# Kernel optimization log

Hardware: AMD Instinct MI355X
Metric: run time of the kernel (lower is better)

The kernel has to match this reference:

```python
import jax, jax.numpy as jnp
import numpy as np

jax.config.update("jax_enable_x64", True)

MANT_SCALE = 8388608.0  # 2**23


def _decode_fp32_bits(bits):
    """[..., 32] {0,1} pulses (MSB-first IEEE-754 float32) -> float64 value."""
    f64 = jnp.float64
    sign = 1.0 - 2.0 * bits[..., 0].astype(f64)
    e = jnp.einsum('...j,j->...', bits[..., 1:9].astype(f64),
                   jnp.exp2(jnp.arange(7, -1, -1, dtype=f64)))
    frac = jnp.einsum('...j,j->...', bits[..., 9:32].astype(f64),
                      jnp.exp2(-jnp.arange(1, 24, dtype=f64)))
    normal = sign * jnp.exp2(e - 127.0) * (1.0 + frac)
    subnorm = sign * jnp.exp2(-126.0) * frac
    return jnp.where(e > 0, normal, subnorm)


def _encode_fp32_bits(y):
    """float64 value already on the fp32 grid -> [..., 32] {0,1} pulses (MSB-first)."""
    f64 = jnp.float64
    sbit = (y < 0).astype(f64)
    a = jnp.abs(y)
    e = jnp.clip(jnp.floor(jnp.log2(jnp.where(a > 0, a, 1.0))), -126.0, 127.0)
    eb = jnp.where(a > 0, e + 127.0, 0.0)          # biased exponent, 0 for zero/subnormal
    frac = jnp.where(eb > 0, a * jnp.exp2(-e) - 1.0, a * jnp.exp2(126.0))
    mant = frac * MANT_SCALE                        # exact integer for fp32-grid y
    ebits = jnp.mod(jnp.floor(eb[..., None] * jnp.exp2(-jnp.arange(7, -1, -1, dtype=f64))), 2.0)
    mbits = jnp.mod(jnp.floor(mant[..., None] * jnp.exp2(-jnp.arange(22, -1, -1, dtype=f64))), 2.0)
    bits = jnp.concatenate([sbit[..., None], ebits, mbits], axis=-1)
    return jnp.where((a > 0)[..., None], bits, 0.0).astype(jnp.float32)


def setup_inputs() -> dict:
    rng = np.random.default_rng(0)
    vals = (rng.standard_normal((1, 2048, 1024)) * 2.0).astype(np.float32)
    words = vals.view(np.uint32)
    shifts = np.arange(31, -1, -1, dtype=np.uint32)
    bits = ((words[..., None] >> shifts) & np.uint32(1)).astype(np.float32)
    return {"x": jnp.asarray(bits)}


def reference(x):
    # GELU(x) ~= x * sigmoid(1.702 * x), all intermediates in fp64 (as the
    # gate-level pipeline does), final result rounded once to fp32 bits.
    xv = _decode_fp32_bits(x)
    y64 = xv * jax.nn.sigmoid(1.702 * xv)
    y32 = y64.astype(jnp.float32).astype(jnp.float64)  # FP64 -> FP32 rounding
    return _encode_fp32_bits(y32)
```

## Files before the change

kernel.cpp:

```cpp
#include <hip/hip_runtime.h>
#include <math.h>


#define LN2C 0x1.62e42fefa39efp-1

typedef unsigned int u32x4 __attribute__((ext_vector_type(4)));

__global__ __launch_bounds__(256) void spike_gelu_kernel(
    const u32x4* __restrict__ in, u32x4* __restrict__ out, int n_vals) {
#pragma clang fp contract(off)
  const double LN2 = LN2C;
  __shared__ double Wdec[8];
  __shared__ double Lms[23];
  __shared__ double E1t[256];
  __shared__ double Vdec[23];
  __shared__ double P2t[254];
  __shared__ uint32_t etab[256];

  const int tid = threadIdx.x;
  if (tid < 8) Wdec[tid] = exp((double)(7 - tid) * LN2);
  if (tid >= 31 && tid < 54) Lms[tid - 31] = exp((double)(31 - tid) * LN2);
  __syncthreads();

  const int lane = tid & 63;
  const int vbase = blockIdx.x * 512 + (tid >> 6) * 128;
  const int n_chunks = n_vals * 8;
  const int cbase = vbase * 8 + lane;
  u32x4 bufA[8];
#pragma unroll
  for (int i = 0; i < 8; ++i) {
    int g = cbase + i * 64;
    u32x4 b = {0u, 0u, 0u, 0u};
    if (g < n_chunks) b = __builtin_nontemporal_load(&in[g]);
    bufA[i] = b;
  }

  if (tid == 0) {
    E1t[0] = exp(-126.0 * LN2);
  } else {
    double e_c = 0.0;
#pragma unroll
    for (int j = 0; j < 8; ++j)
      if ((tid >> (7 - j)) & 1) e_c = e_c + Wdec[j];
    E1t[tid] = exp((e_c - 127.0) * LN2);
  }
  if (tid < 23) Vdec[tid] = exp((double)(-1 - tid) * LN2);
  if (tid < 254) P2t[tid] = exp((double)(126 - tid) * LN2);
  if (tid >= 1 && tid < 255) {
    double eb = (double)tid;
    uint32_t r = 0;
#pragma unroll
    for (int sc = 7; sc >= 0; --sc) {
      double f = floor(eb * Lms[sc]);
      double md = f - 2.0 * floor(0.5 * f);
      r |= ((uint32_t)md) << (23 + sc);
    }
    etab[tid] = r;
  } else {
    etab[tid] = 0u;
  }
  __syncthreads();

  u32x4 bufB[8];
#pragma unroll
  for (int i = 0; i < 8; ++i) {
    int g = cbase + 512 + i * 64;
    u32x4 b = {0u, 0u, 0u, 0u};
    if (g < n_chunks) b = __builtin_nontemporal_load(&in[g]);
    bufB[i] = b;
  }

  const int nibshift = 28 - 4 * (lane & 7);
  const int keep = lane & 7;
  uint32_t w0 = 0u, w1 = 0u;
#pragma unroll
  for (int i = 0; i < 8; ++i) {
    u32x4 b = bufA[i];
    uint32_t p = (((((b.x >> 23) & 1u) << 3) | (((b.y >> 23) & 1u) << 2) |
                   (((b.z >> 23) & 1u) << 1) | ((b.w >> 23) & 1u)))
                 << nibshift;
    p |= __shfl_xor(p, 1);
    p |= __shfl_xor(p, 2);
    p |= __shfl_xor(p, 4);
    if (keep == i) w0 = p;
  }
#pragma unroll
  for (int i = 0; i < 8; ++i) {
    u32x4 b = bufB[i];
    uint32_t p = (((((b.x >> 23) & 1u) << 3) | (((b.y >> 23) & 1u) << 2) |
                   (((b.z >> 23) & 1u) << 1) | ((b.w >> 23) & 1u)))
                 << nibshift;
    p |= __shfl_xor(p, 1);
    p |= __shfl_xor(p, 2);
    p |= __shfl_xor(p, 4);
    if (keep == i) w1 = p;
  }

  const int v0 = vbase + (lane & 7) * 8 + (lane >> 3);
  const int v1 = v0 + 64;
  const bool ok0 = v0 < n_vals, ok1 = v1 < n_vals;

  double f0 = 0.0, f1 = 0.0;
#pragma unroll
  for (int j = 0; j < 23; ++j) {
    double vj = Vdec[j];
    if ((w0 >> (22 - j)) & 1u) f0 = f0 + vj;
    if ((w1 >> (22 - j)) & 1u) f1 = f1 + vj;
  }
  uint32_t ei0 = (w0 >> 23) & 0xFFu, ei1 = (w1 >> 23) & 0xFFu;
  double sg0 = (w0 >> 31) ? -1.0 : 1.0, sg1 = (w1 >> 31) ? -1.0 : 1.0;
  double fa0 = ei0 ? (1.0 + f0) : f0, fa1 = ei1 ? (1.0 + f1) : f1;
  double x0 = (sg0 * E1t[ei0]) * fa0, x1 = (sg1 * E1t[ei1]) * fa1;

  double t0 = 1.702 * x0, t1 = 1.702 * x1;
  double e0v = exp(-t0), e1v = exp(-t1);
  double s0 = 1.0 / (1.0 + e0v), s1 = 1.0 / (1.0 + e1v);
  double y0 = x0 * s0, y1 = x1 * s1;
  float yf0 = (float)y0, yf1 = (float)y1;
  double yd0 = (double)yf0, yd1 = (double)yf1;

  double a0 = fabs(yd0), a1 = fabs(yd1);
  uint32_t yb0 = __float_as_uint(yf0), yb1 = __float_as_uint(yf1);
  uint32_t Ef0 = (yb0 >> 23) & 0xFFu, Ef1 = (yb1 >> 23) & 0xFFu;
  uint32_t mbf0 = yb0 & 0x7FFFFFu, mbf1 = yb1 & 0x7FFFFFu;
  int e00 = (Ef0 == 0u) ? -126 : (int)Ef0 - 127;
  int e01 = (Ef1 == 0u) ? -126 : (int)Ef1 - 127;
  bool pw0 = ok0 && (a0 > 0.0) && (Ef0 != 0u) && (mbf0 == 0u);
  bool pw1 = ok1 && (a1 > 0.0) && (Ef1 != 0u) && (mbf1 == 0u);
  if (__builtin_expect(pw0 || pw1, 0)) {
    if (pw0) {
      double e0 = floor(log(a0) / LN2);
      e00 = (int)fmin(fmax(e0, -126.0), 127.0);
    }
    if (pw1) {
      double e0 = floor(log(a1) / LN2);
      e01 = (int)fmin(fmax(e0, -126.0), 127.0);
    }
  }
  double p20 = P2t[e00 + 126], p21 = P2t[e01 + 126];
  double m10 = a0 * p20, m11 = a1 * p21;
  double mant0 = (m10 - 1.0) * 8388608.0;
  double mant1 = (m11 - 1.0) * 8388608.0;
  int M0 = (int)rint(mant0), M1 = (int)rint(mant1);
  uint32_t mb0 = ((uint32_t)M0) & 0x7FFFFFu, mb1 = ((uint32_t)M1) & 0x7FFFFFu;
  int T0 = M0 ? __builtin_ctz((uint32_t)M0) : 23;
  int T1 = M1 ? __builtin_ctz((uint32_t)M1) : 23;
  int L0 = T0 < 22 ? T0 : 22, L1 = T1 < 22 ? T1 : 22;
  int Lmax = L0 > L1 ? L0 : L1;
  for (int sc = 0; sc <= Lmax; ++sc) {
    double lm = Lms[sc];
    if (sc <= L0) {
      double f = floor(mant0 * lm);
      mb0 = (mb0 & ~(1u << sc)) | (((uint32_t)(((int)f) & 1)) << sc);
    }
    if (sc <= L1) {
      double f = floor(mant1 * lm);
      mb1 = (mb1 & ~(1u << sc)) | (((uint32_t)(((int)f) & 1)) << sc);
    }
  }
  uint32_t ob0 = (yb0 & 0x80000000u) | etab[e00 + 127] | mb0;
  uint32_t ob1 = (yb1 & 0x80000000u) | etab[e01 + 127] | mb1;
  ob0 = (ok0 && a0 > 0.0) ? ob0 : 0u;
  ob1 = (ok1 && a1 > 0.0) ? ob1 : 0u;

#pragma unroll
  for (int i = 0; i < 8; ++i) {
    int g0 = cbase + i * 64;
    int g1 = g0 + 512;
    int src = (lane & 56) + i;
    uint32_t wa = __shfl(ob0, src);
    uint32_t wb = __shfl(ob1, src);
    int base = 31 - 4 * (lane & 7);
    if (g0 < n_chunks) {
      u32x4 o;
      o.x = ((wa >> base) & 1u) * 0x3F800000u;
      o.y = ((wa >> (base - 1)) & 1u) * 0x3F800000u;
      o.z = ((wa >> (base - 2)) & 1u) * 0x3F800000u;
      o.w = ((wa >> (base - 3)) & 1u) * 0x3F800000u;
      __builtin_nontemporal_store(o, &out[g0]);
    }
    if (g1 < n_chunks) {
      u32x4 o;
      o.x = ((wb >> base) & 1u) * 0x3F800000u;
      o.y = ((wb >> (base - 1)) & 1u) * 0x3F800000u;
      o.z = ((wb >> (base - 2)) & 1u) * 0x3F800000u;
      o.w = ((wb >> (base - 3)) & 1u) * 0x3F800000u;
      __builtin_nontemporal_store(o, &out[g1]);
    }
  }
}

extern "C" void kernel_launch(void* const* d_in, const int* in_sizes, int n_in,
                              void* d_out, int out_size, void* d_ws, size_t ws_size,
                              hipStream_t stream) {
  int n_vals = in_sizes[0] / 32;
  int grid = (n_vals + 511) / 512;
  spike_gelu_kernel<<<grid, 256, 0, stream>>>(
      (const u32x4*)d_in[0], (u32x4*)d_out, n_vals);
}
```

Measured before the change: 419.3 us.

## Convert to persistent grid-stride kernel with software-pipelined prefetch of next tile

```diff
diff --git a/kernel.cpp b/kernel.cpp
--- a/kernel.cpp
+++ b/kernel.cpp
@@ -6,8 +6,38 @@
 
 typedef unsigned int u32x4 __attribute__((ext_vector_type(4)));
 
+__device__ __forceinline__ void load_group(const u32x4* __restrict__ in,
+                                           int cb, int n_chunks,
+                                           u32x4 (&B)[8]) {
+#pragma unroll
+  for (int i = 0; i < 8; ++i) {
+    int g = cb + i * 64;
+    u32x4 b = {0u, 0u, 0u, 0u};
+    if (g < n_chunks) b = __builtin_nontemporal_load(&in[g]);
+    B[i] = b;
+  }
+}
+
+__device__ __forceinline__ uint32_t pack_group(const u32x4 (&B)[8],
+                                               int nibshift, int keep) {
+  uint32_t w = 0;
+#pragma unroll
+  for (int i = 0; i < 8; ++i) {
+    u32x4 b = B[i];
+    uint32_t p = (((((b.x >> 23) & 1u) << 3) | (((b.y >> 23) & 1u) << 2) |
+                   (((b.z >> 23) & 1u) << 1) | ((b.w >> 23) & 1u)))
+                 << nibshift;
+    p |= __shfl_xor(p, 1);
+    p |= __shfl_xor(p, 2);
+    p |= __shfl_xor(p, 4);
+    if (keep == i) w = p;
+  }
+  return w;
+}
+
 __global__ __launch_bounds__(256) void spike_gelu_kernel(
-    const u32x4* __restrict__ in, u32x4* __restrict__ out, int n_vals) {
+    const u32x4* __restrict__ in, u32x4* __restrict__ out,
+    int n_vals, int n_tiles) {
 #pragma clang fp contract(off)
   const double LN2 = LN2C;
   __shared__ double Wdec[8];
@@ -18,23 +48,21 @@
   __shared__ uint32_t etab[256];
 
   const int tid = threadIdx.x;
+  const int lane = tid & 63;
+  const int wid = tid >> 6;
+  const int n_chunks = n_vals * 8;
+  const int nibshift = 28 - 4 * (lane & 7);
+  const int keep = lane & 7;
+  const int tstep = gridDim.x;
+
+  int tile = blockIdx.x;
+  u32x4 A[8], Bb[8];
+
+  load_group(in, tile * 4096 + wid * 1024 + lane, n_chunks, A);
+
   if (tid < 8) Wdec[tid] = exp((double)(7 - tid) * LN2);
   if (tid >= 31 && tid < 54) Lms[tid - 31] = exp((double)(31 - tid) * LN2);
   __syncthreads();
-
-  const int lane = tid & 63;
-  const int vbase = blockIdx.x * 512 + (tid >> 6) * 128;
-  const int n_chunks = n_vals * 8;
-  const int cbase = vbase * 8 + lane;
-  u32x4 bufA[8];
-#pragma unroll
-  for (int i = 0; i < 8; ++i) {
-    int g = cbase + i * 64;
-    u32x4 b = {0u, 0u, 0u, 0u};
-    if (g < n_chunks) b = __builtin_nontemporal_load(&in[g]);
-    bufA[i] = b;
-  }
-
   if (tid == 0) {
     E1t[0] = exp(-126.0 * LN2);
   } else {
@@ -61,132 +89,123 @@
   }
   __syncthreads();
 
-  u32x4 bufB[8];
-#pragma unroll
-  for (int i = 0; i < 8; ++i) {
-    int g = cbase + 512 + i * 64;
-    u32x4 b = {0u, 0u, 0u, 0u};
-    if (g < n_chunks) b = __builtin_nontemporal_load(&in[g]);
-    bufB[i] = b;
-  }
-
-  const int nibshift = 28 - 4 * (lane & 7);
-  const int keep = lane & 7;
-  uint32_t w0 = 0u, w1 = 0u;
-#pragma unroll
-  for (int i = 0; i < 8; ++i) {
-    u32x4 b = bufA[i];
-    uint32_t p = (((((b.x >> 23) & 1u) << 3) | (((b.y >> 23) & 1u) << 2) |
-                   (((b.z >> 23) & 1u) << 1) | ((b.w >> 23) & 1u)))
-                 << nibshift;
-    p |= __shfl_xor(p, 1);
-    p |= __shfl_xor(p, 2);
-    p |= __shfl_xor(p, 4);
-    if (keep == i) w0 = p;
-  }
-#pragma unroll
-  for (int i = 0; i < 8; ++i) {
-    u32x4 b = bufB[i];
-    uint32_t p = (((((b.x >> 23) & 1u) << 3) | (((b.y >> 23) & 1u) << 2) |
-                   (((b.z >> 23) & 1u) << 1) | ((b.w >> 23) & 1u)))
-                 << nibshift;
-    p |= __shfl_xor(p, 1);
-    p |= __shfl_xor(p, 2);
-    p |= __shfl_xor(p, 4);
-    if (keep == i) w1 = p;
-  }
-
-  const int v0 = vbase + (lane & 7) * 8 + (lane >> 3);
-  const int v1 = v0 + 64;
-  const bool ok0 = v0 < n_vals, ok1 = v1 < n_vals;
-
-  double f0 = 0.0, f1 = 0.0;
-#pragma unroll
-  for (int j = 0; j < 23; ++j) {
-    double vj = Vdec[j];
-    if ((w0 >> (22 - j)) & 1u) f0 = f0 + vj;
-    if ((w1 >> (22 - j)) & 1u) f1 = f1 + vj;
-  }
-  uint32_t ei0 = (w0 >> 23) & 0xFFu, ei1 = (w1 >> 23) & 0xFFu;
-  double sg0 = (w0 >> 31) ? -1.0 : 1.0, sg1 = (w1 >> 31) ? -1.0 : 1.0;
-  double fa0 = ei0 ? (1.0 + f0) : f0, fa1 = ei1 ? (1.0 + f1) : f1;
-  double x0 = (sg0 * E1t[ei0]) * fa0, x1 = (sg1 * E1t[ei1]) * fa1;
-
-  double t0 = 1.702 * x0, t1 = 1.702 * x1;
-  double e0v = exp(-t0), e1v = exp(-t1);
-  double s0 = 1.0 / (1.0 + e0v), s1 = 1.0 / (1.0 + e1v);
-  double y0 = x0 * s0, y1 = x1 * s1;
-  float yf0 = (float)y0, yf1 = (float)y1;
-  double yd0 = (double)yf0, yd1 = (double)yf1;
-
-  double a0 = fabs(yd0), a1 = fabs(yd1);
-  uint32_t yb0 = __float_as_uint(yf0), yb1 = __float_as_uint(yf1);
-  uint32_t Ef0 = (yb0 >> 23) & 0xFFu, Ef1 = (yb1 >> 23) & 0xFFu;
-  uint32_t mbf0 = yb0 & 0x7FFFFFu, mbf1 = yb1 & 0x7FFFFFu;
-  int e00 = (Ef0 == 0u) ? -126 : (int)Ef0 - 127;
-  int e01 = (Ef1 == 0u) ? -126 : (int)Ef1 - 127;
-  bool pw0 = ok0 && (a0 > 0.0) && (Ef0 != 0u) && (mbf0 == 0u);
-  bool pw1 = ok1 && (a1 > 0.0) && (Ef1 != 0u) && (mbf1 == 0u);
-  if (__builtin_expect(pw0 || pw1, 0)) {
-    if (pw0) {
-      double e0 = floor(log(a0) / LN2);
-      e00 = (int)fmin(fmax(e0, -126.0), 127.0);
-    }
-    if (pw1) {
-      double e0 = floor(log(a1) / LN2);
-      e01 = (int)fmin(fmax(e0, -126.0), 127.0);
-    }
-  }
-  double p20 = P2t[e00 + 126], p21 = P2t[e01 + 126];
-  double m10 = a0 * p20, m11 = a1 * p21;
-  double mant0 = (m10 - 1.0) * 8388608.0;
-  double mant1 = (m11 - 1.0) * 8388608.0;
-  int M0 = (int)rint(mant0), M1 = (int)rint(mant1);
-  uint32_t mb0 = ((uint32_t)M0) & 0x7FFFFFu, mb1 = ((uint32_t)M1) & 0x7FFFFFu;
-  int T0 = M0 ? __builtin_ctz((uint32_t)M0) : 23;
-  int T1 = M1 ? __builtin_ctz((uint32_t)M1) : 23;
-  int L0 = T0 < 22 ? T0 : 22, L1 = T1 < 22 ? T1 : 22;
-  int Lmax = L0 > L1 ? L0 : L1;
-  for (int sc = 0; sc <= Lmax; ++sc) {
-    double lm = Lms[sc];
-    if (sc <= L0) {
-      double f = floor(mant0 * lm);
-      mb0 = (mb0 & ~(1u << sc)) | (((uint32_t)(((int)f) & 1)) << sc);
-    }
-    if (sc <= L1) {
-      double f = floor(mant1 * lm);
-      mb1 = (mb1 & ~(1u << sc)) | (((uint32_t)(((int)f) & 1)) << sc);
-    }
-  }
-  uint32_t ob0 = (yb0 & 0x80000000u) | etab[e00 + 127] | mb0;
-  uint32_t ob1 = (yb1 & 0x80000000u) | etab[e01 + 127] | mb1;
-  ob0 = (ok0 && a0 > 0.0) ? ob0 : 0u;
-  ob1 = (ok1 && a1 > 0.0) ? ob1 : 0u;
-
-#pragma unroll
-  for (int i = 0; i < 8; ++i) {
-    int g0 = cbase + i * 64;
-    int g1 = g0 + 512;
-    int src = (lane & 56) + i;
-    uint32_t wa = __shfl(ob0, src);
-    uint32_t wb = __shfl(ob1, src);
-    int base = 31 - 4 * (lane & 7);
-    if (g0 < n_chunks) {
-      u32x4 o;
-      o.x = ((wa >> base) & 1u) * 0x3F800000u;
-      o.y = ((wa >> (base - 1)) & 1u) * 0x3F800000u;
-      o.z = ((wa >> (base - 2)) & 1u) * 0x3F800000u;
-      o.w = ((wa >> (base - 3)) & 1u) * 0x3F800000u;
-      __builtin_nontemporal_store(o, &out[g0]);
-    }
-    if (g1 < n_chunks) {
-      u32x4 o;
-      o.x = ((wb >> base) & 1u) * 0x3F800000u;
-      o.y = ((wb >> (base - 1)) & 1u) * 0x3F800000u;
-      o.z = ((wb >> (base - 2)) & 1u) * 0x3F800000u;
-      o.w = ((wb >> (base - 3)) & 1u) * 0x3F800000u;
-      __builtin_nontemporal_store(o, &out[g1]);
-    }
+  load_group(in, tile * 4096 + wid * 1024 + lane + 512, n_chunks, Bb);
+  uint32_t w0 = pack_group(A, nibshift, keep);
+  uint32_t w1 = pack_group(Bb, nibshift, keep);
+
+  for (;;) {
+    const int ntile = tile + tstep;
+    const bool havenext = ntile < n_tiles;
+    const int ncb = ntile * 4096 + wid * 1024 + lane;
+    if (havenext) load_group(in, ncb, n_chunks, A);
+
+    const int vbase = tile * 512 + wid * 128;
+    const int v0 = vbase + (lane & 7) * 8 + (lane >> 3);
+    const int v1 = v0 + 64;
+    const bool ok0 = v0 < n_vals, ok1 = v1 < n_vals;
+
+    double f0 = 0.0, f1 = 0.0;
+#pragma unroll
+    for (int j = 0; j < 23; ++j) {
+      double vj = Vdec[j];
+      if ((w0 >> (22 - j)) & 1u) f0 = f0 + vj;
+      if ((w1 >> (22 - j)) & 1u) f1 = f1 + vj;
+    }
+    uint32_t ei0 = (w0 >> 23) & 0xFFu, ei1 = (w1 >> 23) & 0xFFu;
+    double sg0 = (w0 >> 31) ? -1.0 : 1.0, sg1 = (w1 >> 31) ? -1.0 : 1.0;
+    double fa0 = ei0 ? (1.0 + f0) : f0, fa1 = ei1 ? (1.0 + f1) : f1;
+    double x0 = (sg0 * E1t[ei0]) * fa0, x1 = (sg1 * E1t[ei1]) * fa1;
+
+    double t0 = 1.702 * x0, t1 = 1.702 * x1;
+    double e0v = exp(-t0), e1v = exp(-t1);
+    double s0 = 1.0 / (1.0 + e0v), s1 = 1.0 / (1.0 + e1v);
+    double y0 = x0 * s0, y1 = x1 * s1;
+    float yf0 = (float)y0, yf1 = (float)y1;
+    double yd0 = (double)yf0, yd1 = (double)yf1;
+
+    uint32_t nw0 = 0;
+    if (havenext) {
+      nw0 = pack_group(A, nibshift, keep);
+      load_group(in, ncb + 512, n_chunks, Bb);
+    }
+
+    double a0 = fabs(yd0), a1 = fabs(yd1);
+    uint32_t yb0 = __float_as_uint(yf0), yb1 = __float_as_uint(yf1);
+    uint32_t Ef0 = (yb0 >> 23) & 0xFFu, Ef1 = (yb1 >> 23) & 0xFFu;
+    uint32_t mbf0 = yb0 & 0x7FFFFFu, mbf1 = yb1 & 0x7FFFFFu;
+    int e00 = (Ef0 == 0u) ? -126 : (int)Ef0 - 127;
+    int e01 = (Ef1 == 0u) ? -126 : (int)Ef1 - 127;
+    bool pw0 = ok0 && (a0 > 0.0) && (Ef0 != 0u) && (mbf0 == 0u);
+    bool pw1 = ok1 && (a1 > 0.0) && (Ef1 != 0u) && (mbf1 == 0u);
+    if (__builtin_expect(pw0 || pw1, 0)) {
+      if (pw0) {
+        double e0 = floor(log(a0) / LN2);
+        e00 = (int)fmin(fmax(e0, -126.0), 127.0);
+      }
+      if (pw1) {
+        double e0 = floor(log(a1) / LN2);
+        e01 = (int)fmin(fmax(e0, -126.0), 127.0);
+      }
+    }
+    double p20 = P2t[e00 + 126], p21 = P2t[e01 + 126];
+    double m10 = a0 * p20, m11 = a1 * p21;
+    double mant0 = (m10 - 1.0) * 8388608.0;
+    double mant1 = (m11 - 1.0) * 8388608.0;
+    int M0 = (int)rint(mant0), M1 = (int)rint(mant1);
+    uint32_t mb0 = ((uint32_t)M0) & 0x7FFFFFu;
+    uint32_t mb1 = ((uint32_t)M1) & 0x7FFFFFu;
+    int T0 = M0 ? __builtin_ctz((uint32_t)M0) : 23;
+    int T1 = M1 ? __builtin_ctz((uint32_t)M1) : 23;
+    int L0 = T0 < 22 ? T0 : 22, L1 = T1 < 22 ? T1 : 22;
+    int Lmax = L0 > L1 ? L0 : L1;
+    for (int sc = 0; sc <= Lmax; ++sc) {
+      double lm = Lms[sc];
+      if (sc <= L0) {
+        double f = floor(mant0 * lm);
+        mb0 = (mb0 & ~(1u << sc)) | (((uint32_t)(((int)f) & 1)) << sc);
+      }
+      if (sc <= L1) {
+        double f = floor(mant1 * lm);
+        mb1 = (mb1 & ~(1u << sc)) | (((uint32_t)(((int)f) & 1)) << sc);
+      }
+    }
+    uint32_t ob0 = (yb0 & 0x80000000u) | etab[e00 + 127] | mb0;
+    uint32_t ob1 = (yb1 & 0x80000000u) | etab[e01 + 127] | mb1;
+    ob0 = (ok0 && a0 > 0.0) ? ob0 : 0u;
+    ob1 = (ok1 && a1 > 0.0) ? ob1 : 0u;
+
+    const int ccb = tile * 4096 + wid * 1024 + lane;
+#pragma unroll
+    for (int i = 0; i < 8; ++i) {
+      int g0 = ccb + i * 64;
+      int g1 = g0 + 512;
+      int src = (lane & 56) + i;
+      uint32_t wa = __shfl(ob0, src);
+      uint32_t wb = __shfl(ob1, src);
+      int base = 31 - 4 * (lane & 7);
+      if (g0 < n_chunks) {
+        u32x4 o;
+        o.x = ((wa >> base) & 1u) * 0x3F800000u;
+        o.y = ((wa >> (base - 1)) & 1u) * 0x3F800000u;
+        o.z = ((wa >> (base - 2)) & 1u) * 0x3F800000u;
+        o.w = ((wa >> (base - 3)) & 1u) * 0x3F800000u;
+        __builtin_nontemporal_store(o, &out[g0]);
+      }
+      if (g1 < n_chunks) {
+        u32x4 o;
+        o.x = ((wb >> base) & 1u) * 0x3F800000u;
+        o.y = ((wb >> (base - 1)) & 1u) * 0x3F800000u;
+        o.z = ((wb >> (base - 2)) & 1u) * 0x3F800000u;
+        o.w = ((wb >> (base - 3)) & 1u) * 0x3F800000u;
+        __builtin_nontemporal_store(o, &out[g1]);
+      }
+    }
+
+    if (!havenext) break;
+    uint32_t nw1 = pack_group(Bb, nibshift, keep);
+    w0 = nw0;
+    w1 = nw1;
+    tile = ntile;
   }
 }
 
@@ -194,7 +213,8 @@
                               void* d_out, int out_size, void* d_ws, size_t ws_size,
                               hipStream_t stream) {
   int n_vals = in_sizes[0] / 32;
-  int grid = (n_vals + 511) / 512;
+  int n_tiles = (n_vals + 511) / 512;
+  int grid = n_tiles < 1024 ? n_tiles : 1024;
   spike_gelu_kernel<<<grid, 256, 0, stream>>>(
-      (const u32x4*)d_in[0], (u32x4*)d_out, n_vals);
-}
+      (const u32x4*)d_in[0], (u32x4*)d_out, n_vals, n_tiles);
+}
```

Result: no change. 423.2 us (+0.9%).

## Use 512-thread blocks with one value per lane to raise occupancy

Applied to the files above, without the earlier changes.

```diff
diff --git a/kernel.cpp b/kernel.cpp
--- a/kernel.cpp
+++ b/kernel.cpp
@@ -6,7 +6,7 @@
 
 typedef unsigned int u32x4 __attribute__((ext_vector_type(4)));
 
-__global__ __launch_bounds__(256) void spike_gelu_kernel(
+__global__ __launch_bounds__(512, 6) void spike_gelu_kernel(
     const u32x4* __restrict__ in, u32x4* __restrict__ out, int n_vals) {
 #pragma clang fp contract(off)
   const double LN2 = LN2C;
@@ -18,26 +18,28 @@
   __shared__ uint32_t etab[256];
 
   const int tid = threadIdx.x;
-  if (tid < 8) Wdec[tid] = exp((double)(7 - tid) * LN2);
-  if (tid >= 31 && tid < 54) Lms[tid - 31] = exp((double)(31 - tid) * LN2);
-  __syncthreads();
+  const int lane = tid & 63;
+  const int wid = tid >> 6;
+  const int n_chunks = n_vals * 8;
 
-  const int lane = tid & 63;
-  const int vbase = blockIdx.x * 512 + (tid >> 6) * 128;
-  const int n_chunks = n_vals * 8;
-  const int cbase = vbase * 8 + lane;
-  u32x4 bufA[8];
+  const int vwave = blockIdx.x * 512 + wid * 64;
+  const int cbase = vwave * 8 + lane;
+
+  u32x4 A[8];
 #pragma unroll
   for (int i = 0; i < 8; ++i) {
     int g = cbase + i * 64;
     u32x4 b = {0u, 0u, 0u, 0u};
     if (g < n_chunks) b = __builtin_nontemporal_load(&in[g]);
-    bufA[i] = b;
+    A[i] = b;
   }
 
+  if (tid < 8) Wdec[tid] = exp((double)(7 - tid) * LN2);
+  if (tid >= 31 && tid < 54) Lms[tid - 31] = exp((double)(31 - tid) * LN2);
+  __syncthreads();
   if (tid == 0) {
     E1t[0] = exp(-126.0 * LN2);
-  } else {
+  } else if (tid < 256) {
     double e_c = 0.0;
 #pragma unroll
     for (int j = 0; j < 8; ++j)
@@ -46,36 +48,30 @@
   }
   if (tid < 23) Vdec[tid] = exp((double)(-1 - tid) * LN2);
   if (tid < 254) P2t[tid] = exp((double)(126 - tid) * LN2);
-  if (tid >= 1 && tid < 255) {
-    double eb = (double)tid;
-    uint32_t r = 0;
+  if (tid >= 256) {
+    const int tt = tid - 256;
+    if (tt >= 1 && tt < 255) {
+      double eb = (double)tt;
+      uint32_t r = 0;
 #pragma unroll
-    for (int sc = 7; sc >= 0; --sc) {
-      double f = floor(eb * Lms[sc]);
-      double md = f - 2.0 * floor(0.5 * f);
-      r |= ((uint32_t)md) << (23 + sc);
+      for (int sc = 7; sc >= 0; --sc) {
+        double f = floor(eb * Lms[sc]);
+        double md = f - 2.0 * floor(0.5 * f);
+        r |= ((uint32_t)md) << (23 + sc);
+      }
+      etab[tt] = r;
+    } else {
+      etab[tt] = 0u;
     }
-    etab[tid] = r;
-  } else {
-    etab[tid] = 0u;
   }
   __syncthreads();
 
-  u32x4 bufB[8];
+  const int nibshift = 28 - 4 * (lane & 7);
+  const int keep = lane & 7;
+  uint32_t w0 = 0u;
 #pragma unroll
   for (int i = 0; i < 8; ++i) {
-    int g = cbase + 512 + i * 64;
-    u32x4 b = {0u, 0u, 0u, 0u};
-    if (g < n_chunks) b = __builtin_nontemporal_load(&in[g]);
-    bufB[i] = b;
-  }
-
-  const int nibshift = 28 - 4 * (lane & 7);
-  const int keep = lane & 7;
-  uint32_t w0 = 0u, w1 = 0u;
-#pragma unroll
-  for (int i = 0; i < 8; ++i) {
-    u32x4 b = bufA[i];
+    u32x4 b = A[i];
     uint32_t p = (((((b.x >> 23) & 1u) << 3) | (((b.y >> 23) & 1u) << 2) |
                    (((b.z >> 23) & 1u) << 1) | ((b.w >> 23) & 1u)))
                  << nibshift;
@@ -84,108 +80,65 @@
     p |= __shfl_xor(p, 4);
     if (keep == i) w0 = p;
   }
+
+  const int v0 = vwave + (lane & 7) * 8 + (lane >> 3);
+  const bool ok0 = v0 < n_vals;
+
+  double f0 = 0.0;
+#pragma unroll
+  for (int j = 0; j < 23; ++j)
+    if ((w0 >> (22 - j)) & 1u) f0 = f0 + Vdec[j];
+  uint32_t ei0 = (w0 >> 23) & 0xFFu;
+  double sg0 = (w0 >> 31) ? -1.0 : 1.0;
+  double fa0 = ei0 ? (1.0 + f0) : f0;
+  double x0 = (sg0 * E1t[ei0]) * fa0;
+
+  double t0 = 1.702 * x0;
+  double e0v = exp(-t0);
+  double s0 = 1.0 / (1.0 + e0v);
+  double y0 = x0 * s0;
+  float yf0 = (float)y0;
+  double yd0 = (double)yf0;
+
+  double a0 = fabs(yd0);
+  uint32_t yb0 = __float_as_uint(yf0);
+  uint32_t Ef0 = (yb0 >> 23) & 0xFFu;
+  uint32_t mbf0 = yb0 & 0x7FFFFFu;
+  int e00 = (Ef0 == 0u) ? -126 : (int)Ef0 - 127;
+  bool pw0 = ok0 && (a0 > 0.0) && (Ef0 != 0u) && (mbf0 == 0u);
+  if (__builtin_expect(pw0, 0)) {
+    double e0 = floor(log(a0) / LN2);
+    e00 = (int)fmin(fmax(e0, -126.0), 127.0);
+  }
+  double p20 = P2t[e00 + 126];
+  double m10 = a0 * p20;
+  double mant0 = (m10 - 1.0) * 8388608.0;
+  int M0 = (int)rint(mant0);
+  uint32_t mb0 = ((uint32_t)M0) & 0x7FFFFFu;
+  int T0 = M0 ? __builtin_ctz((uint32_t)M0) : 23;
+  int L0 = T0 < 22 ? T0 : 22;
+  for (int sc = 0; sc <= L0; ++sc) {
+    double f = floor(mant0 * Lms[sc]);
+    mb0 = (mb0 & ~(1u << sc)) | (((uint32_t)(((int)f) & 1)) << sc);
+  }
+  uint32_t ob0 = (yb0 & 0x80000000u) | etab[e00 + 127] | mb0;
+  ob0 = (ok0 && a0 > 0.0) ? ob0 : 0u;
+
+  uint32_t wv[8];
+#pragma unroll
+  for (int i = 0; i < 8; ++i) wv[i] = __shfl(ob0, (lane & 56) + i);
+  const int base = 31 - 4 * (lane & 7);
 #pragma unroll
   for (int i = 0; i < 8; ++i) {
-    u32x4 b = bufB[i];
-    uint32_t p = (((((b.x >> 23) & 1u) << 3) | (((b.y >> 23) & 1u) << 2) |
-                   (((b.z >> 23) & 1u) << 1) | ((b.w >> 23) & 1u)))
-                 << nibshift;
-    p |= __shfl_xor(p, 1);
-    p |= __shfl_xor(p, 2);
-    p |= __shfl_xor(p, 4);
-    if (keep == i) w1 = p;
-  }
-
-  const int v0 = vbase + (lane & 7) * 8 + (lane >> 3);
-  const int v1 = v0 + 64;
-  const bool ok0 = v0 < n_vals, ok1 = v1 < n_vals;
-
-  double f0 = 0.0, f1 = 0.0;
-#pragma unroll
-  for (int j = 0; j < 23; ++j) {
-    double vj = Vdec[j];
-    if ((w0 >> (22 - j)) & 1u) f0 = f0 + vj;
-    if ((w1 >> (22 - j)) & 1u) f1 = f1 + vj;
-  }
-  uint32_t ei0 = (w0 >> 23) & 0xFFu, ei1 = (w1 >> 23) & 0xFFu;
-  double sg0 = (w0 >> 31) ? -1.0 : 1.0, sg1 = (w1 >> 31) ? -1.0 : 1.0;
-  double fa0 = ei0 ? (1.0 + f0) : f0, fa1 = ei1 ? (1.0 + f1) : f1;
-  double x0 = (sg0 * E1t[ei0]) * fa0, x1 = (sg1 * E1t[ei1]) * fa1;
-
-  double t0 = 1.702 * x0, t1 = 1.702 * x1;
-  double e0v = exp(-t0), e1v = exp(-t1);
-  double s0 = 1.0 / (1.0 + e0v), s1 = 1.0 / (1.0 + e1v);
-  double y0 = x0 * s0, y1 = x1 * s1;
-  float yf0 = (float)y0, yf1 = (float)y1;
-  double yd0 = (double)yf0, yd1 = (double)yf1;
-
-  double a0 = fabs(yd0), a1 = fabs(yd1);
-  uint32_t yb0 = __float_as_uint(yf0), yb1 = __float_as_uint(yf1);
-  uint32_t Ef0 = (yb0 >> 23) & 0xFFu, Ef1 = (yb1 >> 23) & 0xFFu;
-  uint32_t mbf0 = yb0 & 0x7FFFFFu, mbf1 = yb1 & 0x7FFFFFu;
-  int e00 = (Ef0 == 0u) ? -126 : (int)Ef0 - 127;
-  int e01 = (Ef1 == 0u) ? -126 : (int)Ef1 - 127;
-  bool pw0 = ok0 && (a0 > 0.0) && (Ef0 != 0u) && (mbf0 == 0u);
-  bool pw1 = ok1 && (a1 > 0.0) && (Ef1 != 0u) && (mbf1 == 0u);
-  if (__builtin_expect(pw0 || pw1, 0)) {
-    if (pw0) {
-      double e0 = floor(log(a0) / LN2);
-      e00 = (int)fmin(fmax(e0, -126.0), 127.0);
-    }
-    if (pw1) {
-      double e0 = floor(log(a1) / LN2);
-      e01 = (int)fmin(fmax(e0, -126.0), 127.0);
-    }
-  }
-  double p20 = P2t[e00 + 126], p21 = P2t[e01 + 126];
-  double m10 = a0 * p20, m11 = a1 * p21;
-  double mant0 = (m10 - 1.0) * 8388608.0;
-  double mant1 = (m11 - 1.0) * 8388608.0;
-  int M0 = (int)rint(mant0), M1 = (int)rint(mant1);
-  uint32_t mb0 = ((uint32_t)M0) & 0x7FFFFFu, mb1 = ((uint32_t)M1) & 0x7FFFFFu;
-  int T0 = M0 ? __builtin_ctz((uint32_t)M0) : 23;
-  int T1 = M1 ? __builtin_ctz((uint32_t)M1) : 23;
-  int L0 = T0 < 22 ? T0 : 22, L1 = T1 < 22 ? T1 : 22;
-  int Lmax = L0 > L1 ? L0 : L1;
-  for (int sc = 0; sc <= Lmax; ++sc) {
-    double lm = Lms[sc];
-    if (sc <= L0) {
-      double f = floor(mant0 * lm);
-      mb0 = (mb0 & ~(1u << sc)) | (((uint32_t)(((int)f) & 1)) << sc);
-    }
-    if (sc <= L1) {
-      double f = floor(mant1 * lm);
-      mb1 = (mb1 & ~(1u << sc)) | (((uint32_t)(((int)f) & 1)) << sc);
-    }
-  }
-  uint32_t ob0 = (yb0 & 0x80000000u) | etab[e00 + 127] | mb0;
-  uint32_t ob1 = (yb1 & 0x80000000u) | etab[e01 + 127] | mb1;
-  ob0 = (ok0 && a0 > 0.0) ? ob0 : 0u;
-  ob1 = (ok1 && a1 > 0.0) ? ob1 : 0u;
-
-#pragma unroll
-  for (int i = 0; i < 8; ++i) {
-    int g0 = cbase + i * 64;
-    int g1 = g0 + 512;
-    int src = (lane & 56) + i;
-    uint32_t wa = __shfl(ob0, src);
-    uint32_t wb = __shfl(ob1, src);
-    int base = 31 - 4 * (lane & 7);
-    if (g0 < n_chunks) {
+    int g = cbase + i * 64;
+    if (g < n_chunks) {
+      uint32_t wa = wv[i];
       u32x4 o;
       o.x = ((wa >> base) & 1u) * 0x3F800000u;
       o.y = ((wa >> (base - 1)) & 1u) * 0x3F800000u;
       o.z = ((wa >> (base - 2)) & 1u) * 0x3F800000u;
       o.w = ((wa >> (base - 3)) & 1u) * 0x3F800000u;
-      __builtin_nontemporal_store(o, &out[g0]);
-    }
-    if (g1 < n_chunks) {
-      u32x4 o;
-      o.x = ((wb >> base) & 1u) * 0x3F800000u;
-      o.y = ((wb >> (base - 1)) & 1u) * 0x3F800000u;
-      o.z = ((wb >> (base - 2)) & 1u) * 0x3F800000u;
-      o.w = ((wb >> (base - 3)) & 1u) * 0x3F800000u;
-      __builtin_nontemporal_store(o, &out[g1]);
+      __builtin_nontemporal_store(o, &out[g]);
     }
   }
 }
@@ -195,6 +148,6 @@
                               hipStream_t stream) {
   int n_vals = in_sizes[0] / 32;
   int grid = (n_vals + 511) / 512;
-  spike_gelu_kernel<<<grid, 256, 0, stream>>>(
+  spike_gelu_kernel<<<grid, 512, 0, stream>>>(
       (const u32x4*)d_in[0], (u32x4*)d_out, n_vals);
 }
```

After: 418.9 us. Within noise of the previous version (-0.1%).
